# Kernel tuning notes

Measured on AMD Instinct MI355X. Metric: run time of the kernel, lower is better.

The kernel has to match this reference:

```python
import jax, jax.numpy as jnp
import numpy as np

# --- configuration constants (match init_kwargs) ---
N = 256          # num_oscillators
T = 200          # simulation steps
INTERVAL = 5     # readout_update_interval
OFFSET = 1       # spike_update_offset
DELAY = 10
D = DELAY + 1    # delay-buffer length
K_GLOBAL = 1.0   # global_coupling_strength
STEP_SIZE = 0.1
GAMMA_ATTR = 0.5 # gamma_attraction_strength
DECAY = 0.9      # membrane_decay
THRESH = 1.0
REC_SCALE = 0.1
ALPHA_FIX = 0.5  # fixed_alpha_value (fixed during training)
CLS_START = 50   # classifier_start_step
SURR_BETA = 4.0  # surrogate-gradient sharpness
NUM_CLASSES = 10


def _spike(u):
    # Heaviside forward, sigmoid surrogate backward (straight-through)
    sg = jax.nn.sigmoid(SURR_BETA * u)
    hard = (u > 0).astype(u.dtype)
    return sg + jax.lax.stop_gradient(hard - sg)


def _forward(x, theta0, W_init, omega, W_ro, W_gate, W_rec, W_fb, W_cls, b_cls):
    B = x.shape[0]
    P = W_gate.shape[1]  # num_pixels = H*W*C
    xf = x.reshape(B, -1)
    gamma0 = jnp.tanh(xf @ W_init)                 # ReadoutLayer.initialize_gamma_from_input -> [B,N]
    buf0 = jnp.tile(theta0[None], (D, 1, 1))       # theta delay buffer [D,B,N]
    zN = jnp.zeros((B, N), x.dtype)
    zP = jnp.zeros((B, P), x.dtype)
    carry0 = (theta0, gamma0, zN, zP, zP, zN, buf0)  # theta, gamma, gate, membrane, spikes, fb-activity a, buffer

    def step(carry, s):
        theta, gamma, gate, mem, spk, a, buf = carry
        # --- KuramotoLayer: dtheta_i = omega_i + K/N * sum_j (1 + W_ij*alpha) sin(th_j - th_i) + attr*gamma_i
        # top-down connectivity W_ij = a_i a_j is rank-1, so the coupling sum is computed exactly in O(N).
        sin_t = jnp.sin(theta); cos_t = jnp.cos(theta)
        S = sin_t.sum(-1, keepdims=True); C = cos_t.sum(-1, keepdims=True)
        base = cos_t * S - sin_t * C
        as_ = jnp.sum(a * sin_t, -1, keepdims=True)
        ac_ = jnp.sum(a * cos_t, -1, keepdims=True)
        weighted = ALPHA_FIX * (cos_t * a * as_ - sin_t * a * ac_)
        dtheta = omega + (K_GLOBAL / N) * (base + weighted) + GAMMA_ATTR * gamma
        theta = theta + STEP_SIZE * dtheta

        # --- ReadoutLayer.gamma_update + SinusoidalGate every INTERVAL steps
        def ro_upd(args):
            g = jnp.tanh(theta @ W_ro)
            gt = g * 0.5 * (1.0 + jnp.cos(theta - buf[0]))  # gate from delayed phase difference
            return g, gt
        gamma, gate = jax.lax.cond((s % INTERVAL) == 0, ro_upd, lambda args: args, (gamma, gate))

        # --- SNNLayer.forward_step + TopDownFeedback on offset spike-update steps
        def sp_upd(args):
            mem_, spk_, a_ = args
            cur = gate @ W_gate + REC_SCALE * (spk_ @ W_rec)
            mem_ = DECAY * mem_ * (1.0 - spk_) + cur       # leaky membrane with reset
            spk_ = _spike(mem_ - THRESH)
            a_ = jnp.tanh(spk_ @ W_fb)                     # per-oscillator feedback activity
            return mem_, spk_, a_
        m_sp = (((s - OFFSET) % INTERVAL) == 0) & (s > OFFSET)
        mem, spk, a = jax.lax.cond(m_sp, sp_upd, lambda args: args, (mem, spk, a))

        buf = jnp.concatenate([buf[1:], theta[None]], axis=0)
        return (theta, gamma, gate, mem, spk, a, buf), spk

    _, spk_hist = jax.lax.scan(step, carry0, jnp.arange(1, T + 1))
    spike_trace = jnp.transpose(spk_hist, (1, 0, 2))       # [B,T,P]
    rate = jnp.mean(spike_trace[:, CLS_START:, :], axis=1) # SNNLayer.classify: mean firing rate
    logits = rate @ W_cls + b_cls
    return logits


def setup_inputs() -> dict:
    key = jax.random.key(0)
    ks = jax.random.split(key, 10)
    B, H, W, C = 32, 32, 32, 3
    P = H * W * C
    x = jax.random.normal(ks[0], (B, H, W, C), jnp.float32)
    theta0 = jax.random.normal(ks[1], (B, N), jnp.float32)
    W_init = jax.random.normal(ks[2], (P, N), jnp.float32) / np.sqrt(P).astype(np.float32)
    omega = jax.random.normal(ks[3], (N,), jnp.float32) * 0.5
    W_ro = jax.random.normal(ks[4], (N, N), jnp.float32) / np.sqrt(N).astype(np.float32)
    W_gate = jax.random.normal(ks[5], (N, P), jnp.float32) / np.sqrt(N).astype(np.float32)
    W_rec = jax.random.normal(ks[6], (P, P), jnp.float32) / np.sqrt(P).astype(np.float32)
    W_fb = jax.random.normal(ks[7], (P, N), jnp.float32) / np.sqrt(P).astype(np.float32)
    W_cls = jax.random.normal(ks[8], (P, NUM_CLASSES), jnp.float32) / np.sqrt(P).astype(np.float32)
    b_cls = jnp.zeros((NUM_CLASSES,), jnp.float32)
    return dict(x=x, theta0=theta0, W_init=W_init, omega=omega, W_ro=W_ro,
                W_gate=W_gate, W_rec=W_rec, W_fb=W_fb, W_cls=W_cls, b_cls=b_cls)


def reference(x, theta0, W_init, omega, W_ro, W_gate, W_rec, W_fb, W_cls, b_cls):
    return _forward(x, theta0, W_init, omega, W_ro, W_gate, W_rec, W_fb, W_cls, b_cls)
```

## Files before the change

kernel.cpp:

```cpp
#include <hip/hip_runtime.h>
#include <cstdint>
#include <cstddef>

#define BB 32
#define NN 256
#define PP 3072
#define NG 192
#define RING 16

typedef unsigned short u16;

__global__ __launch_bounds__(512) void k_init(
    const float* __restrict__ x, const float* __restrict__ W_init,
    double* __restrict__ gpartI, double* __restrict__ memD,
    double* __restrict__ a_g, float* __restrict__ rate,
    u16* __restrict__ maskA, u16* __restrict__ maskB) {
  const int blk = blockIdx.x, tid = threadIdx.x;
  if (blk < 192) {
    const int b = blk / 6, sub = blk % 6;
    __shared__ double xl[512];
    xl[tid] = (double)x[(size_t)b * PP + sub * 512 + tid];
    __syncthreads();
    const int osc = tid & 255, kh = tid >> 8;
    const float* wp = W_init + (size_t)(sub * 512 + kh * 256) * NN + osc;
    const double* xp = xl + kh * 256;
    double a0 = 0, a1 = 0, a2 = 0, a3 = 0, a4 = 0, a5 = 0, a6 = 0, a7 = 0;
    for (int r = 0; r < 256; r += 8) {
      a0 += xp[r + 0] * (double)wp[(size_t)(r + 0) * NN];
      a1 += xp[r + 1] * (double)wp[(size_t)(r + 1) * NN];
      a2 += xp[r + 2] * (double)wp[(size_t)(r + 2) * NN];
      a3 += xp[r + 3] * (double)wp[(size_t)(r + 3) * NN];
      a4 += xp[r + 4] * (double)wp[(size_t)(r + 4) * NN];
      a5 += xp[r + 5] * (double)wp[(size_t)(r + 5) * NN];
      a6 += xp[r + 6] * (double)wp[(size_t)(r + 6) * NN];
      a7 += xp[r + 7] * (double)wp[(size_t)(r + 7) * NN];
    }
    double acc = ((a0 + a1) + (a2 + a3)) + ((a4 + a5) + (a6 + a7));
    __syncthreads();
    __shared__ double hl[256];
    if (kh) hl[osc] = acc;
    __syncthreads();
    if (!kh) gpartI[((size_t)b * 6 + sub) * 256 + osc] = acc + hl[osc];
  } else {
    const int b = blk - 192;
    for (int i = tid; i < PP; i += 512) {
      memD[(size_t)b * PP + i] = 0.0;
      rate[(size_t)b * PP + i] = 0.f;
    }
    for (int i = tid; i < NG; i += 512) {
      maskA[b * NG + i] = 0;
      maskB[b * NG + i] = 0;
    }
    for (int i = tid; i < NN; i += 512) a_g[b * NN + i] = 0.0;
  }
}

__global__ __launch_bounds__(512, 6) void k_rec(
    const float* __restrict__ W_rec, const u16* __restrict__ listG,
    const int* __restrict__ cntG, const int* __restrict__ cntB,
    double* __restrict__ recPart, const double* __restrict__ gateG,
    const float* __restrict__ W_gate, double* __restrict__ gatePart) {
  __shared__ double gd[16 * 130];
  __shared__ float wt[128 * 16];
  __shared__ double red[256];
  const int g = blockIdx.x, bh = blockIdx.y, z = blockIdx.z, j0 = g * 16;
  const int tid = threadIdx.x;

  if (z < 3) {
    const int qd = tid & 3;
    const int h = (tid >> 2) & 7;
    const int bl = tid >> 5;
    const int b = bh * 16 + bl;
    const int beg = (z == 0) ? 0 : cntB[b * 2 + (z - 1)];
    const int end = (z == 2) ? cntG[b] : cntB[b * 2 + z];
    const u16* lst = listG + (size_t)b * PP;
    const float* wp = W_rec + j0 + 4 * qd;

    double a0 = 0, a1 = 0, a2 = 0, a3 = 0;
    int i = beg + h;
    for (; i + 32 <= end; i += 32) {
      const int r0 = lst[i], r1 = lst[i + 8], r2 = lst[i + 16],
                r3 = lst[i + 24];
      const float4 f0 = *(const float4*)(wp + (size_t)r0 * PP);
      const float4 f1 = *(const float4*)(wp + (size_t)r1 * PP);
      const float4 f2 = *(const float4*)(wp + (size_t)r2 * PP);
      const float4 f3 = *(const float4*)(wp + (size_t)r3 * PP);
      a0 += (double)f0.x; a1 += (double)f0.y;
      a2 += (double)f0.z; a3 += (double)f0.w;
      a0 += (double)f1.x; a1 += (double)f1.y;
      a2 += (double)f1.z; a3 += (double)f1.w;
      a0 += (double)f2.x; a1 += (double)f2.y;
      a2 += (double)f2.z; a3 += (double)f2.w;
      a0 += (double)f3.x; a1 += (double)f3.y;
      a2 += (double)f3.z; a3 += (double)f3.w;
    }
    for (; i < end; i += 8) {
      const float4 f = *(const float4*)(wp + (size_t)lst[i] * PP);
      a0 += (double)f.x; a1 += (double)f.y;
      a2 += (double)f.z; a3 += (double)f.w;
    }
    a0 += __shfl_xor(a0, 4); a0 += __shfl_xor(a0, 8); a0 += __shfl_xor(a0, 16);
    a1 += __shfl_xor(a1, 4); a1 += __shfl_xor(a1, 8); a1 += __shfl_xor(a1, 16);
    a2 += __shfl_xor(a2, 4); a2 += __shfl_xor(a2, 8); a2 += __shfl_xor(a2, 16);
    a3 += __shfl_xor(a3, 4); a3 += __shfl_xor(a3, 8); a3 += __shfl_xor(a3, 16);
    if (h == 0) {
      double* dst = recPart + ((size_t)z * BB + b) * PP + j0 + 4 * qd;
      dst[0] = a0; dst[1] = a1; dst[2] = a2; dst[3] = a3;
    }
  } else {
    const int zh = z - 3;
    for (int i = tid; i < 2048; i += 512) {
      gd[(i >> 7) * 130 + (i & 127)] =
          gateG[(size_t)(bh * 16 + (i >> 7)) * 256 + zh * 128 + (i & 127)];
      wt[i] = W_gate[(size_t)(zh * 128 + (i >> 4)) * PP + j0 + (i & 15)];
    }
    __syncthreads();
    const int pi = tid & 15, bl = (tid >> 4) & 15, hq = tid >> 8;
    const int b = bh * 16 + bl, p = j0 + pi, pid = tid & 255;
    double s0 = 0, s1 = 0, s2 = 0, s3 = 0, s4 = 0, s5 = 0, s6 = 0, s7 = 0;
    const double* gq = gd + bl * 130 + hq * 64;
    const float* wq = wt + hq * 64 * 16 + pi;
    for (int k = 0; k < 64; k += 8) {
      s0 += gq[k + 0] * (double)wq[(k + 0) * 16];
      s1 += gq[k + 1] * (double)wq[(k + 1) * 16];
      s2 += gq[k + 2] * (double)wq[(k + 2) * 16];
      s3 += gq[k + 3] * (double)wq[(k + 3) * 16];
      s4 += gq[k + 4] * (double)wq[(k + 4) * 16];
      s5 += gq[k + 5] * (double)wq[(k + 5) * 16];
      s6 += gq[k + 6] * (double)wq[(k + 6) * 16];
      s7 += gq[k + 7] * (double)wq[(k + 7) * 16];
    }
    double vg = ((s0 + s1) + (s2 + s3)) + ((s4 + s5) + (s6 + s7));
    if (hq) red[pid] = vg;
    __syncthreads();
    if (!hq) gatePart[((size_t)zh * BB + b) * PP + p] = vg + red[pid];
  }
}

__global__ __launch_bounds__(512) void k_fin(
    const u16* __restrict__ mask_rd, u16* __restrict__ mask_wr,
    double* __restrict__ memD, const double* __restrict__ gatePart,
    const double* __restrict__ recPart, float* __restrict__ rate, int accum) {
  const int g = blockIdx.x, tid = threadIdx.x;
  const int pi = tid & 15, b = tid >> 4;
  const int p = g * 16 + pi;
  const size_t idx = (size_t)b * PP + p;
  const double vgs = gatePart[idx] + gatePart[(size_t)BB * PP + idx];
  const double vrs = (recPart[idx] + recPart[(size_t)BB * PP + idx]) +
                     recPart[(size_t)2 * BB * PP + idx];
  const double cur = vgs + 0.1 * vrs;
  const double so = (double)((mask_rd[b * NG + g] >> pi) & 1);
  const double mv = 0.9 * memD[idx] * (1.0 - so) + cur;
  const double sv = (mv - 1.0 > 0.0) ? 1.0 : 0.0;
  memD[idx] = mv;
  if (accum) rate[idx] += (float)sv;
  unsigned long long bal = __ballot(sv > 0.5);
  const int lane = tid & 63;
  if ((lane & 15) == 0)
    mask_wr[b * NG + g] = (u16)((bal >> (16 * (lane >> 4))) & 0xFFFFull);
}

__global__ __launch_bounds__(256) void k_fb(
    const u16* __restrict__ spk_mask, u16* __restrict__ listG,
    int* __restrict__ cntG, int* __restrict__ cntB,
    const float* __restrict__ W_fb, double* __restrict__ a_part) {
  const int b = blockIdx.x, y = blockIdx.y, tid = threadIdx.x;
  __shared__ int pc[NG], sc[NG];
  __shared__ u16 m_l[NG];
  __shared__ u16 list_l[PP];
  if (tid < NG) {
    m_l[tid] = spk_mask[b * NG + tid];
    pc[tid] = __popc((unsigned int)m_l[tid]);
    sc[tid] = pc[tid];
  }
  __syncthreads();
  for (int d = 1; d < NG; d <<= 1) {
    int v = 0;
    if (tid < NG) v = sc[tid] + ((tid >= d) ? sc[tid - d] : 0);
    __syncthreads();
    if (tid < NG) sc[tid] = v;
    __syncthreads();
  }
  const int total = sc[NG - 1];
  if (tid < NG) {
    int off = sc[tid] - pc[tid];
    unsigned int m = m_l[tid];
    while (m) {
      int bit = __builtin_ctz(m);
      m &= m - 1;
      list_l[off++] = (u16)(tid * 16 + bit);
    }
  }
  __syncthreads();
  if (y == 0) {
    for (int i = tid; i < total; i += 256) listG[(size_t)b * PP + i] = list_l[i];
    if (tid == 0) {
      cntG[b] = total;
      cntB[b * 2 + 0] = sc[63];
      cntB[b * 2 + 1] = sc[127];
    }
  }
  const int j = tid;
  double c0 = 0, c1 = 0, c2 = 0, c3 = 0, c4 = 0, c5 = 0, c6 = 0, c7 = 0;
  int i = y;
  for (; i + 128 <= total; i += 128) {
    c0 += (double)W_fb[(size_t)list_l[i + 0] * NN + j];
    c1 += (double)W_fb[(size_t)list_l[i + 16] * NN + j];
    c2 += (double)W_fb[(size_t)list_l[i + 32] * NN + j];
    c3 += (double)W_fb[(size_t)list_l[i + 48] * NN + j];
    c4 += (double)W_fb[(size_t)list_l[i + 64] * NN + j];
    c5 += (double)W_fb[(size_t)list_l[i + 80] * NN + j];
    c6 += (double)W_fb[(size_t)list_l[i + 96] * NN + j];
    c7 += (double)W_fb[(size_t)list_l[i + 112] * NN + j];
  }
  double acc = ((c0 + c1) + (c2 + c3)) + ((c4 + c5) + (c6 + c7));
  for (; i < total; i += 16) acc += (double)W_fb[(size_t)list_l[i] * NN + j];
  a_part[((size_t)b * 16 + y) * NN + j] = acc;
}

__global__ __launch_bounds__(512) void k_theta(
    double* __restrict__ ring, double* __restrict__ gamma_g,
    double* __restrict__ a_g, double* __restrict__ gateG,
    const double* __restrict__ a_part, const float* __restrict__ theta0,
    const float* __restrict__ omega, const float* __restrict__ W_ro,
    const double* __restrict__ gpartI, int* __restrict__ cntG,
    int* __restrict__ cntB, int k2) {
  const int b = blockIdx.x, tid = threadIdx.x;
  const int j = tid & 255, q = tid >> 8;
  const int lane = tid & 63, wid = tid >> 6;
  __shared__ double th[256];
  __shared__ double red[16];
  __shared__ double qpart[256];

  const int s0 = 5 * k2 + 1, s1 = 5 * k2 + 5;
  double new_a = 0.0;
  if (k2 > 0) {
    double s = 0.0;
#pragma unroll
    for (int u = 0; u < 8; ++u)
      s += a_part[((size_t)b * 16 + q * 8 + u) * NN + j];
    if (q) qpart[j] = s;
    __syncthreads();
    if (!q) new_a = tanh(s + qpart[j]);
    __syncthreads();
  }

  double t = 0.0, aj = 0.0, gm = 0.0, om = 0.0;
  if (!q) {
    om = (double)omega[j];
    if (k2 == 0) {
      double s = 0.0;
      for (int c6 = 0; c6 < 6; ++c6) s += gpartI[((size_t)b * 6 + c6) * 256 + j];
      gm = tanh(s);
      t = (double)theta0[b * NN + j];
      ring[0 * BB * NN + b * NN + j] = t;
      if (tid == 0) {
        cntG[b] = 0;
        cntB[b * 2 + 0] = 0;
        cntB[b * 2 + 1] = 0;
      }
    } else {
      t = ring[((s0 - 1) & (RING - 1)) * BB * NN + b * NN + j];
      aj = a_g[b * NN + j];
      gm = gamma_g[b * NN + j];
    }
  }

  for (int s = s0; s <= s1; ++s) {
    if (!q && k2 > 0 && s == s0 + 1) {
      aj = new_a;
      a_g[b * NN + j] = aj;
    }
    double sn = 0.0, cs = 0.0;
    if (!q) sincos(t, &sn, &cs);
    double r0 = sn, r1 = cs, r2 = aj * sn, r3 = aj * cs;
#pragma unroll
    for (int o = 32; o; o >>= 1) {
      r0 += __shfl_down(r0, o);
      r1 += __shfl_down(r1, o);
      r2 += __shfl_down(r2, o);
      r3 += __shfl_down(r3, o);
    }
    if (lane == 0 && wid < 4) {
      red[wid * 4 + 0] = r0;
      red[wid * 4 + 1] = r1;
      red[wid * 4 + 2] = r2;
      red[wid * 4 + 3] = r3;
    }
    __syncthreads();
    double S = red[0] + red[4] + red[8] + red[12];
    double C = red[1] + red[5] + red[9] + red[13];
    double AS = red[2] + red[6] + red[10] + red[14];
    double AC = red[3] + red[7] + red[11] + red[15];
    __syncthreads();
    if (!q) {
      double base = cs * S - sn * C;
      double wgt = 0.5 * (cs * aj * AS - sn * aj * AC);
      t = t + 0.1 * (om + (1.0 / 256.0) * (base + wgt) + 0.5 * gm);
      ring[(s & (RING - 1)) * BB * NN + b * NN + j] = t;
    }
  }
  if (!q) th[j] = t;
  __syncthreads();
  {
    double c0 = 0, c1 = 0, c2 = 0, c3 = 0, c4 = 0, c5 = 0, c6 = 0, c7 = 0;
    const float* wp = W_ro + j;
    const int i0 = q * 128;
    for (int i = 0; i < 128; i += 8) {
      c0 += th[i0 + i + 0] * (double)wp[(size_t)(i0 + i + 0) * NN];
      c1 += th[i0 + i + 1] * (double)wp[(size_t)(i0 + i + 1) * NN];
      c2 += th[i0 + i + 2] * (double)wp[(size_t)(i0 + i + 2) * NN];
      c3 += th[i0 + i + 3] * (double)wp[(size_t)(i0 + i + 3) * NN];
      c4 += th[i0 + i + 4] * (double)wp[(size_t)(i0 + i + 4) * NN];
      c5 += th[i0 + i + 5] * (double)wp[(size_t)(i0 + i + 5) * NN];
      c6 += th[i0 + i + 6] * (double)wp[(size_t)(i0 + i + 6) * NN];
      c7 += th[i0 + i + 7] * (double)wp[(size_t)(i0 + i + 7) * NN];
    }
    double acc = ((c0 + c1) + (c2 + c3)) + ((c4 + c5) + (c6 + c7));
    if (q) qpart[j] = acc;
    __syncthreads();
    if (!q) {
      double gnew = tanh(acc + qpart[j]);
      gamma_g[b * NN + j] = gnew;
      int sd = s1 - 11;
      if (sd < 0) sd = 0;
      double dly = ring[(sd & (RING - 1)) * BB * NN + b * NN + j];
      double gt = gnew * 0.5 * (1.0 + cos(t - dly));
      gateG[(size_t)b * 256 + j] = gt;
    }
  }
}

__global__ __launch_bounds__(256) void k_cls(const float* __restrict__ rate,
                                             const float* __restrict__ Wcls,
                                             const float* __restrict__ bcls,
                                             float* __restrict__ out) {
  const int b = blockIdx.x, t = threadIdx.x;
  double acc[10];
#pragma unroll
  for (int c = 0; c < 10; ++c) acc[c] = 0.0;
  for (int p = t; p < PP; p += 256) {
    double r = (double)rate[(size_t)b * PP + p] / 30.0;
#pragma unroll
    for (int c = 0; c < 10; ++c) acc[c] += r * (double)Wcls[(size_t)p * 10 + c];
  }
  __shared__ double sh[10][256];
#pragma unroll
  for (int c = 0; c < 10; ++c) sh[c][t] = acc[c];
  __syncthreads();
  for (int off = 128; off; off >>= 1) {
    if (t < off)
#pragma unroll
      for (int c = 0; c < 10; ++c) sh[c][t] += sh[c][t + off];
    __syncthreads();
  }
  if (t < 10) out[b * 10 + t] = (float)(sh[t][0] + (double)bcls[t]);
}

extern "C" void kernel_launch(void* const* d_in, const int* in_sizes, int n_in,
                              void* d_out, int out_size, void* d_ws,
                              size_t ws_size, hipStream_t stream) {
  const float* x = (const float*)d_in[0];
  const float* theta0 = (const float*)d_in[1];
  const float* W_init = (const float*)d_in[2];
  const float* omega = (const float*)d_in[3];
  const float* W_ro = (const float*)d_in[4];
  const float* W_gate = (const float*)d_in[5];
  const float* W_rec = (const float*)d_in[6];
  const float* W_fb = (const float*)d_in[7];
  const float* W_cls = (const float*)d_in[8];
  const float* b_cls = (const float*)d_in[9];

  char* w = (char*)d_ws;
  size_t off = 0;
  auto alloc = [&](size_t sz) -> void* {
    void* p = w + off;
    off = (off + sz + 255) & ~(size_t)255;
    return p;
  };
  double* ring = (double*)alloc((size_t)RING * BB * NN * 8);
  double* gamma = (double*)alloc((size_t)BB * NN * 8);
  double* a_g = (double*)alloc((size_t)BB * NN * 8);
  double* gateG = (double*)alloc((size_t)BB * NN * 8);
  double* memD = (double*)alloc((size_t)BB * PP * 8);
  float* rate = (float*)alloc((size_t)BB * PP * 4);
  u16* maskA = (u16*)alloc((size_t)BB * NG * 2);
  u16* maskB = (u16*)alloc((size_t)BB * NG * 2);
  u16* listG = (u16*)alloc((size_t)BB * PP * 2);
  int* cntG = (int*)alloc((size_t)BB * 4);
  int* cntB = (int*)alloc((size_t)BB * 2 * 4);
  double* gpartI = (double*)alloc((size_t)BB * 6 * 256 * 8);
  double* a_part = (double*)alloc((size_t)BB * 16 * NN * 8);
  double* recPart = (double*)alloc((size_t)3 * BB * PP * 8);
  double* gatePart = (double*)alloc((size_t)2 * BB * PP * 8);

  k_init<<<224, 512, 0, stream>>>(x, W_init, gpartI, memD, a_g, rate, maskA,
                                  maskB);
  k_theta<<<32, 512, 0, stream>>>(ring, gamma, a_g, gateG, a_part, theta0,
                                  omega, W_ro, gpartI, cntG, cntB, 0);
  for (int k = 1; k < 40; ++k) {
    const u16* mrd = (k & 1) ? maskA : maskB;
    u16* mwr = (k & 1) ? maskB : maskA;
    k_rec<<<dim3(192, 2, 5), 512, 0, stream>>>(W_rec, listG, cntG, cntB,
                                               recPart, gateG, W_gate,
                                               gatePart);
    k_fin<<<192, 512, 0, stream>>>(mrd, mwr, memD, gatePart, recPart, rate,
                                   (k >= 10) ? 1 : 0);
    k_fb<<<dim3(32, 16), 256, 0, stream>>>(mwr, listG, cntG, cntB, W_fb,
                                           a_part);
    k_theta<<<32, 512, 0, stream>>>(ring, gamma, a_g, gateG, a_part, theta0,
                                    omega, W_ro, gpartI, cntG, cntB, k);
  }
  k_cls<<<32, 256, 0, stream>>>(rate, W_cls, b_cls, (float*)d_out);
}
```

Measured before the change: 2.115 ms.

## Fuse membrane update, spike feedback and theta step into one per-batch kernel

The membrane/spike finalize kernel, the feedback gather kernel, and the theta kernel are merged into a single 32-block kernel, one block per batch row. This removes two launches per outer step and the a_part global round trip. The cost is far less parallelism: the spike update and the W_fb gather over spiking pixels now run on 32 blocks instead of 192 and 512, and each block's gather is split across only two halves.

```diff
diff --git a/kernel.cpp b/kernel.cpp
--- a/kernel.cpp
+++ b/kernel.cpp
@@ -137,112 +137,102 @@
   }
 }
 
-__global__ __launch_bounds__(512) void k_fin(
+__global__ __launch_bounds__(512) void k_theta2(
+    double* __restrict__ ring, double* __restrict__ gamma_g,
+    double* __restrict__ a_g, double* __restrict__ gateG,
+    const float* __restrict__ theta0, const float* __restrict__ omega,
+    const float* __restrict__ W_ro, const float* __restrict__ W_fb,
+    const double* __restrict__ gpartI, u16* __restrict__ listG,
+    int* __restrict__ cntG, int* __restrict__ cntB,
     const u16* __restrict__ mask_rd, u16* __restrict__ mask_wr,
     double* __restrict__ memD, const double* __restrict__ gatePart,
-    const double* __restrict__ recPart, float* __restrict__ rate, int accum) {
-  const int g = blockIdx.x, tid = threadIdx.x;
-  const int pi = tid & 15, b = tid >> 4;
-  const int p = g * 16 + pi;
-  const size_t idx = (size_t)b * PP + p;
-  const double vgs = gatePart[idx] + gatePart[(size_t)BB * PP + idx];
-  const double vrs = (recPart[idx] + recPart[(size_t)BB * PP + idx]) +
-                     recPart[(size_t)2 * BB * PP + idx];
-  const double cur = vgs + 0.1 * vrs;
-  const double so = (double)((mask_rd[b * NG + g] >> pi) & 1);
-  const double mv = 0.9 * memD[idx] * (1.0 - so) + cur;
-  const double sv = (mv - 1.0 > 0.0) ? 1.0 : 0.0;
-  memD[idx] = mv;
-  if (accum) rate[idx] += (float)sv;
-  unsigned long long bal = __ballot(sv > 0.5);
+    const double* __restrict__ recPart, float* __restrict__ rate, int accum,
+    int k2) {
+  const int b = blockIdx.x, tid = threadIdx.x;
+  const int j = tid & 255, q = tid >> 8;
   const int lane = tid & 63;
-  if ((lane & 15) == 0)
-    mask_wr[b * NG + g] = (u16)((bal >> (16 * (lane >> 4))) & 0xFFFFull);
-}
-
-__global__ __launch_bounds__(256) void k_fb(
-    const u16* __restrict__ spk_mask, u16* __restrict__ listG,
-    int* __restrict__ cntG, int* __restrict__ cntB,
-    const float* __restrict__ W_fb, double* __restrict__ a_part) {
-  const int b = blockIdx.x, y = blockIdx.y, tid = threadIdx.x;
+  const int wid = tid >> 6;
+  __shared__ double th[256];
+  __shared__ double red[16];
+  __shared__ double qpart[256];
   __shared__ int pc[NG], sc[NG];
   __shared__ u16 m_l[NG];
   __shared__ u16 list_l[PP];
-  if (tid < NG) {
-    m_l[tid] = spk_mask[b * NG + tid];
-    pc[tid] = __popc((unsigned int)m_l[tid]);
-    sc[tid] = pc[tid];
-  }
-  __syncthreads();
-  for (int d = 1; d < NG; d <<= 1) {
-    int v = 0;
-    if (tid < NG) v = sc[tid] + ((tid >= d) ? sc[tid - d] : 0);
-    __syncthreads();
-    if (tid < NG) sc[tid] = v;
-    __syncthreads();
-  }
-  const int total = sc[NG - 1];
-  if (tid < NG) {
-    int off = sc[tid] - pc[tid];
-    unsigned int m = m_l[tid];
-    while (m) {
-      int bit = __builtin_ctz(m);
-      m &= m - 1;
-      list_l[off++] = (u16)(tid * 16 + bit);
-    }
-  }
-  __syncthreads();
-  if (y == 0) {
-    for (int i = tid; i < total; i += 256) listG[(size_t)b * PP + i] = list_l[i];
+
+  const int s0 = 5 * k2 + 1, s1 = 5 * k2 + 5;
+  double new_a = 0.0;
+
+  if (k2 > 0) {
+    for (int c = 0; c < 6; ++c) {
+      const int p = c * 512 + tid;
+      const int g = p >> 4;
+      const size_t idx = (size_t)b * PP + p;
+      const double vgs = gatePart[idx] + gatePart[(size_t)BB * PP + idx];
+      const double vrs = (recPart[idx] + recPart[(size_t)BB * PP + idx]) +
+                         recPart[(size_t)2 * BB * PP + idx];
+      const double cur = vgs + 0.1 * vrs;
+      const double so = (double)((mask_rd[b * NG + g] >> (p & 15)) & 1);
+      const double mv = 0.9 * memD[idx] * (1.0 - so) + cur;
+      const double sv = (mv - 1.0 > 0.0) ? 1.0 : 0.0;
+      memD[idx] = mv;
+      if (accum) rate[idx] += (float)sv;
+      unsigned long long bal = __ballot(sv > 0.5);
+      if ((lane & 15) == 0)
+        m_l[g] = (u16)((bal >> (16 * (lane >> 4))) & 0xFFFFull);
+    }
+    __syncthreads();
+    for (int i = tid; i < NG; i += 512) mask_wr[b * NG + i] = m_l[i];
+
+    if (tid < NG) {
+      pc[tid] = __popc((unsigned int)m_l[tid]);
+      sc[tid] = pc[tid];
+    }
+    __syncthreads();
+    for (int d = 1; d < NG; d <<= 1) {
+      int v = 0;
+      if (tid < NG) v = sc[tid] + ((tid >= d) ? sc[tid - d] : 0);
+      __syncthreads();
+      if (tid < NG) sc[tid] = v;
+      __syncthreads();
+    }
+    const int total = sc[NG - 1];
+    if (tid < NG) {
+      int off = sc[tid] - pc[tid];
+      unsigned int m = m_l[tid];
+      while (m) {
+        int bit = __builtin_ctz(m);
+        m &= m - 1;
+        list_l[off++] = (u16)(tid * 16 + bit);
+      }
+    }
+    __syncthreads();
+    for (int i = tid; i < total; i += 512) listG[(size_t)b * PP + i] = list_l[i];
     if (tid == 0) {
       cntG[b] = total;
       cntB[b * 2 + 0] = sc[63];
       cntB[b * 2 + 1] = sc[127];
     }
-  }
-  const int j = tid;
-  double c0 = 0, c1 = 0, c2 = 0, c3 = 0, c4 = 0, c5 = 0, c6 = 0, c7 = 0;
-  int i = y;
-  for (; i + 128 <= total; i += 128) {
-    c0 += (double)W_fb[(size_t)list_l[i + 0] * NN + j];
-    c1 += (double)W_fb[(size_t)list_l[i + 16] * NN + j];
-    c2 += (double)W_fb[(size_t)list_l[i + 32] * NN + j];
-    c3 += (double)W_fb[(size_t)list_l[i + 48] * NN + j];
-    c4 += (double)W_fb[(size_t)list_l[i + 64] * NN + j];
-    c5 += (double)W_fb[(size_t)list_l[i + 80] * NN + j];
-    c6 += (double)W_fb[(size_t)list_l[i + 96] * NN + j];
-    c7 += (double)W_fb[(size_t)list_l[i + 112] * NN + j];
-  }
-  double acc = ((c0 + c1) + (c2 + c3)) + ((c4 + c5) + (c6 + c7));
-  for (; i < total; i += 16) acc += (double)W_fb[(size_t)list_l[i] * NN + j];
-  a_part[((size_t)b * 16 + y) * NN + j] = acc;
-}
-
-__global__ __launch_bounds__(512) void k_theta(
-    double* __restrict__ ring, double* __restrict__ gamma_g,
-    double* __restrict__ a_g, double* __restrict__ gateG,
-    const double* __restrict__ a_part, const float* __restrict__ theta0,
-    const float* __restrict__ omega, const float* __restrict__ W_ro,
-    const double* __restrict__ gpartI, int* __restrict__ cntG,
-    int* __restrict__ cntB, int k2) {
-  const int b = blockIdx.x, tid = threadIdx.x;
-  const int j = tid & 255, q = tid >> 8;
-  const int lane = tid & 63, wid = tid >> 6;
-  __shared__ double th[256];
-  __shared__ double red[16];
-  __shared__ double qpart[256];
-
-  const int s0 = 5 * k2 + 1, s1 = 5 * k2 + 5;
-  double new_a = 0.0;
-  if (k2 > 0) {
-    double s = 0.0;
-#pragma unroll
-    for (int u = 0; u < 8; ++u)
-      s += a_part[((size_t)b * 16 + q * 8 + u) * NN + j];
-    if (q) qpart[j] = s;
-    __syncthreads();
-    if (!q) new_a = tanh(s + qpart[j]);
-    __syncthreads();
+
+    {
+      double c0 = 0, c1 = 0, c2 = 0, c3 = 0, c4 = 0, c5 = 0, c6 = 0, c7 = 0;
+      int i = q;
+      for (; i + 16 <= total; i += 16) {
+        c0 += (double)W_fb[(size_t)list_l[i + 0] * NN + j];
+        c1 += (double)W_fb[(size_t)list_l[i + 2] * NN + j];
+        c2 += (double)W_fb[(size_t)list_l[i + 4] * NN + j];
+        c3 += (double)W_fb[(size_t)list_l[i + 6] * NN + j];
+        c4 += (double)W_fb[(size_t)list_l[i + 8] * NN + j];
+        c5 += (double)W_fb[(size_t)list_l[i + 10] * NN + j];
+        c6 += (double)W_fb[(size_t)list_l[i + 12] * NN + j];
+        c7 += (double)W_fb[(size_t)list_l[i + 14] * NN + j];
+      }
+      double acc = ((c0 + c1) + (c2 + c3)) + ((c4 + c5) + (c6 + c7));
+      for (; i < total; i += 2) acc += (double)W_fb[(size_t)list_l[i] * NN + j];
+      if (q) qpart[j] = acc;
+      __syncthreads();
+      if (!q) new_a = tanh(acc + qpart[j]);
+      __syncthreads();
+    }
   }
 
   double t = 0.0, aj = 0.0, gm = 0.0, om = 0.0;
@@ -390,26 +380,25 @@
   int* cntG = (int*)alloc((size_t)BB * 4);
   int* cntB = (int*)alloc((size_t)BB * 2 * 4);
   double* gpartI = (double*)alloc((size_t)BB * 6 * 256 * 8);
-  double* a_part = (double*)alloc((size_t)BB * 16 * NN * 8);
   double* recPart = (double*)alloc((size_t)3 * BB * PP * 8);
   double* gatePart = (double*)alloc((size_t)2 * BB * PP * 8);
 
   k_init<<<224, 512, 0, stream>>>(x, W_init, gpartI, memD, a_g, rate, maskA,
                                   maskB);
-  k_theta<<<32, 512, 0, stream>>>(ring, gamma, a_g, gateG, a_part, theta0,
-                                  omega, W_ro, gpartI, cntG, cntB, 0);
+  k_theta2<<<32, 512, 0, stream>>>(ring, gamma, a_g, gateG, theta0, omega,
+                                   W_ro, W_fb, gpartI, listG, cntG, cntB,
+                                   maskA, maskB, memD, gatePart, recPart, rate,
+                                   0, 0);
   for (int k = 1; k < 40; ++k) {
     const u16* mrd = (k & 1) ? maskA : maskB;
     u16* mwr = (k & 1) ? maskB : maskA;
     k_rec<<<dim3(192, 2, 5), 512, 0, stream>>>(W_rec, listG, cntG, cntB,
                                                recPart, gateG, W_gate,
                                                gatePart);
-    k_fin<<<192, 512, 0, stream>>>(mrd, mwr, memD, gatePart, recPart, rate,
-                                   (k >= 10) ? 1 : 0);
-    k_fb<<<dim3(32, 16), 256, 0, stream>>>(mwr, listG, cntG, cntB, W_fb,
-                                           a_part);
-    k_theta<<<32, 512, 0, stream>>>(ring, gamma, a_g, gateG, a_part, theta0,
-                                    omega, W_ro, gpartI, cntG, cntB, k);
+    k_theta2<<<32, 512, 0, stream>>>(ring, gamma, a_g, gateG, theta0, omega,
+                                     W_ro, W_fb, gpartI, listG, cntG, cntB,
+                                     mrd, mwr, memD, gatePart, recPart, rate,
+                                     (k >= 10) ? 1 : 0, k);
   }
   k_cls<<<32, 256, 0, stream>>>(rate, W_cls, b_cls, (float*)d_out);
 }
```

Result: slower. 2.565 ms (+21.3%).

## Fuse per-interval kernels into one persistent cooperative kernel with grid syncs

Applied to the files above, without the earlier changes.

Replaces the 39-iteration loop of four kernel launches with a single cooperative persistent kernel that uses grid-wide syncs between phases. The W_gate tile is kept resident in shared memory across iterations. The recurrent gather is split into 16 even slices and overlapped with the theta/readout phase on the other blocks. This removes launch overhead and per-launch reloads, at the cost of grid-sync latency, higher shared-memory use and dependence on enough co-resident blocks; the old multi-kernel path remains as a fallback.

```diff
diff --git a/kernel.cpp b/kernel.cpp
--- a/kernel.cpp
+++ b/kernel.cpp
@@ -1,12 +1,18 @@
 #include <hip/hip_runtime.h>
+#include <hip/hip_cooperative_groups.h>
 #include <cstdint>
 #include <cstddef>
+
+namespace cg = cooperative_groups;
 
 #define BB 32
 #define NN 256
 #define PP 3072
 #define NG 192
 #define RING 16
+#define SREC 16
+#define NBLK 768
+#define NGATH 736
 
 typedef unsigned short u16;
 
@@ -14,7 +20,8 @@
     const float* __restrict__ x, const float* __restrict__ W_init,
     double* __restrict__ gpartI, double* __restrict__ memD,
     double* __restrict__ a_g, float* __restrict__ rate,
-    u16* __restrict__ maskA, u16* __restrict__ maskB) {
+    u16* __restrict__ maskA, u16* __restrict__ maskB, int* __restrict__ cntG,
+    int* __restrict__ cntB) {
   const int blk = blockIdx.x, tid = threadIdx.x;
   if (blk < 192) {
     const int b = blk / 6, sub = blk % 6;
@@ -52,6 +59,268 @@
       maskB[b * NG + i] = 0;
     }
     for (int i = tid; i < NN; i += 512) a_g[b * NN + i] = 0.0;
+    if (tid == 0) {
+      cntG[b] = 0;
+      cntB[b * 2 + 0] = 0;
+      cntB[b * 2 + 1] = 0;
+    }
+  }
+}
+
+__global__ __launch_bounds__(512, 6) void k_mega(
+    double* __restrict__ ring, double* __restrict__ gamma_g,
+    double* __restrict__ a_g, double* __restrict__ gateG,
+    const float* __restrict__ theta0, const float* __restrict__ omega,
+    const float* __restrict__ W_ro, const float* __restrict__ W_fb,
+    const double* __restrict__ gpartI, u16* __restrict__ listG,
+    int* __restrict__ cntG, u16* __restrict__ maskA, u16* __restrict__ maskB,
+    double* __restrict__ memD, const float* __restrict__ W_rec,
+    const float* __restrict__ W_gate, double* __restrict__ recPart,
+    double* __restrict__ a_part, float* __restrict__ rate) {
+  cg::grid_group grd = cg::this_grid();
+  const int blk = blockIdx.x, tid = threadIdx.x;
+  const int lane = tid & 63, wid = tid >> 6;
+  __shared__ float wt[256 * 16];
+  __shared__ int pc[NG], sc[NG];
+  __shared__ u16 m_l[NG];
+  __shared__ u16 list_l[PP];
+  __shared__ double th[256];
+  __shared__ double redp[16];
+  __shared__ double qpart[256];
+
+  if (blk < 192) {
+    for (int i = tid; i < 4096; i += 512)
+      wt[i] = W_gate[(size_t)(i >> 4) * PP + blk * 16 + (i & 15)];
+    __syncthreads();
+  }
+
+  for (int k = 0; k < 40; ++k) {
+    const u16* mrd = (k & 1) ? maskA : maskB;
+    u16* mwr = (k & 1) ? maskB : maskA;
+    if (k > 0) {
+      if (blk < 192) {
+        const int g = blk, pi = tid & 15, bl = tid >> 4;
+        const size_t idx = (size_t)bl * PP + g * 16 + pi;
+        double s0 = 0, s1 = 0, s2 = 0, s3 = 0, s4 = 0, s5 = 0, s6 = 0, s7 = 0;
+        const double* gq = gateG + bl * 256;
+        const float* wq = wt + pi;
+        for (int kk = 0; kk < 256; kk += 8) {
+          s0 += gq[kk + 0] * (double)wq[(kk + 0) * 16];
+          s1 += gq[kk + 1] * (double)wq[(kk + 1) * 16];
+          s2 += gq[kk + 2] * (double)wq[(kk + 2) * 16];
+          s3 += gq[kk + 3] * (double)wq[(kk + 3) * 16];
+          s4 += gq[kk + 4] * (double)wq[(kk + 4) * 16];
+          s5 += gq[kk + 5] * (double)wq[(kk + 5) * 16];
+          s6 += gq[kk + 6] * (double)wq[(kk + 6) * 16];
+          s7 += gq[kk + 7] * (double)wq[(kk + 7) * 16];
+        }
+        const double vg = ((s0 + s1) + (s2 + s3)) + ((s4 + s5) + (s6 + s7));
+        double vrs = 0.0;
+        for (int s = 0; s < SREC; ++s) vrs += recPart[(size_t)s * BB * PP + idx];
+        const double cur = vg + 0.1 * vrs;
+        const double so = (double)((mrd[bl * NG + g] >> pi) & 1);
+        const double mv = 0.9 * memD[idx] * (1.0 - so) + cur;
+        const double sv = (mv - 1.0 > 0.0) ? 1.0 : 0.0;
+        memD[idx] = mv;
+        if (k >= 10) rate[idx] += (float)sv;
+        unsigned long long bal = __ballot(sv > 0.5);
+        if ((lane & 15) == 0)
+          mwr[bl * NG + g] = (u16)((bal >> (16 * (lane >> 4))) & 0xFFFFull);
+      }
+      grd.sync();
+      if (blk < 512) {
+        const int b = blk >> 4, y = blk & 15;
+        if (tid < NG) {
+          m_l[tid] = mwr[b * NG + tid];
+          pc[tid] = __popc((unsigned int)m_l[tid]);
+          sc[tid] = pc[tid];
+        }
+        __syncthreads();
+        for (int d = 1; d < NG; d <<= 1) {
+          int v = 0;
+          if (tid < NG) v = sc[tid] + ((tid >= d) ? sc[tid - d] : 0);
+          __syncthreads();
+          if (tid < NG) sc[tid] = v;
+          __syncthreads();
+        }
+        const int total = sc[NG - 1];
+        if (tid < NG) {
+          int off = sc[tid] - pc[tid];
+          unsigned int m = m_l[tid];
+          while (m) {
+            int bit = __builtin_ctz(m);
+            m &= m - 1;
+            list_l[off++] = (u16)(tid * 16 + bit);
+          }
+        }
+        __syncthreads();
+        if (y == 0) {
+          for (int i = tid; i < total; i += 512)
+            listG[(size_t)b * PP + i] = list_l[i];
+          if (tid == 0) cntG[b] = total;
+        }
+        if (tid < 256) {
+          const int j = tid;
+          double c0 = 0, c1 = 0, c2 = 0, c3 = 0, c4 = 0, c5 = 0, c6 = 0,
+                 c7 = 0;
+          int i = y;
+          for (; i + 128 <= total; i += 128) {
+            c0 += (double)W_fb[(size_t)list_l[i + 0] * NN + j];
+            c1 += (double)W_fb[(size_t)list_l[i + 16] * NN + j];
+            c2 += (double)W_fb[(size_t)list_l[i + 32] * NN + j];
+            c3 += (double)W_fb[(size_t)list_l[i + 48] * NN + j];
+            c4 += (double)W_fb[(size_t)list_l[i + 64] * NN + j];
+            c5 += (double)W_fb[(size_t)list_l[i + 80] * NN + j];
+            c6 += (double)W_fb[(size_t)list_l[i + 96] * NN + j];
+            c7 += (double)W_fb[(size_t)list_l[i + 112] * NN + j];
+          }
+          double acc = ((c0 + c1) + (c2 + c3)) + ((c4 + c5) + (c6 + c7));
+          for (; i < total; i += 16)
+            acc += (double)W_fb[(size_t)list_l[i] * NN + j];
+          a_part[((size_t)b * 16 + y) * NN + j] = acc;
+        }
+      }
+      grd.sync();
+    }
+    if (blk < 32) {
+      const int b = blk;
+      const int j = tid & 255, q = tid >> 8;
+      const int s0 = 5 * k + 1, s1 = 5 * k + 5;
+      double new_a = 0.0;
+      if (k > 0) {
+        double s = 0.0;
+#pragma unroll
+        for (int u = 0; u < 8; ++u)
+          s += a_part[((size_t)b * 16 + q * 8 + u) * NN + j];
+        if (q) qpart[j] = s;
+        __syncthreads();
+        if (!q) new_a = tanh(s + qpart[j]);
+        __syncthreads();
+      }
+      double t = 0.0, aj = 0.0, gm = 0.0, om = 0.0;
+      if (!q) {
+        om = (double)omega[j];
+        if (k == 0) {
+          double s = 0.0;
+          for (int c6 = 0; c6 < 6; ++c6)
+            s += gpartI[((size_t)b * 6 + c6) * 256 + j];
+          gm = tanh(s);
+          t = (double)theta0[b * NN + j];
+          ring[0 * BB * NN + b * NN + j] = t;
+        } else {
+          t = ring[((s0 - 1) & (RING - 1)) * BB * NN + b * NN + j];
+          aj = a_g[b * NN + j];
+          gm = gamma_g[b * NN + j];
+        }
+      }
+      for (int s = s0; s <= s1; ++s) {
+        if (!q && k > 0 && s == s0 + 1) {
+          aj = new_a;
+          a_g[b * NN + j] = aj;
+        }
+        double sn = 0.0, cs = 0.0;
+        if (!q) sincos(t, &sn, &cs);
+        double r0 = sn, r1 = cs, r2 = aj * sn, r3 = aj * cs;
+#pragma unroll
+        for (int o = 32; o; o >>= 1) {
+          r0 += __shfl_down(r0, o);
+          r1 += __shfl_down(r1, o);
+          r2 += __shfl_down(r2, o);
+          r3 += __shfl_down(r3, o);
+        }
+        if (lane == 0 && wid < 4) {
+          redp[wid * 4 + 0] = r0;
+          redp[wid * 4 + 1] = r1;
+          redp[wid * 4 + 2] = r2;
+          redp[wid * 4 + 3] = r3;
+        }
+        __syncthreads();
+        double S = redp[0] + redp[4] + redp[8] + redp[12];
+        double C = redp[1] + redp[5] + redp[9] + redp[13];
+        double AS = redp[2] + redp[6] + redp[10] + redp[14];
+        double AC = redp[3] + redp[7] + redp[11] + redp[15];
+        __syncthreads();
+        if (!q) {
+          double base = cs * S - sn * C;
+          double wgt = 0.5 * (cs * aj * AS - sn * aj * AC);
+          t = t + 0.1 * (om + (1.0 / 256.0) * (base + wgt) + 0.5 * gm);
+          ring[(s & (RING - 1)) * BB * NN + b * NN + j] = t;
+        }
+      }
+      if (!q) th[j] = t;
+      __syncthreads();
+      {
+        double c0 = 0, c1 = 0, c2 = 0, c3 = 0, c4 = 0, c5 = 0, c6 = 0, c7 = 0;
+        const float* wp = W_ro + j;
+        const int i0 = q * 128;
+        for (int i = 0; i < 128; i += 8) {
+          c0 += th[i0 + i + 0] * (double)wp[(size_t)(i0 + i + 0) * NN];
+          c1 += th[i0 + i + 1] * (double)wp[(size_t)(i0 + i + 1) * NN];
+          c2 += th[i0 + i + 2] * (double)wp[(size_t)(i0 + i + 2) * NN];
+          c3 += th[i0 + i + 3] * (double)wp[(size_t)(i0 + i + 3) * NN];
+          c4 += th[i0 + i + 4] * (double)wp[(size_t)(i0 + i + 4) * NN];
+          c5 += th[i0 + i + 5] * (double)wp[(size_t)(i0 + i + 5) * NN];
+          c6 += th[i0 + i + 6] * (double)wp[(size_t)(i0 + i + 6) * NN];
+          c7 += th[i0 + i + 7] * (double)wp[(size_t)(i0 + i + 7) * NN];
+        }
+        double acc = ((c0 + c1) + (c2 + c3)) + ((c4 + c5) + (c6 + c7));
+        if (q) qpart[j] = acc;
+        __syncthreads();
+        if (!q) {
+          double gnew = tanh(acc + qpart[j]);
+          gamma_g[b * NN + j] = gnew;
+          int sd = s1 - 11;
+          if (sd < 0) sd = 0;
+          double dly = ring[(sd & (RING - 1)) * BB * NN + b * NN + j];
+          double gt = gnew * 0.5 * (1.0 + cos(t - dly));
+          gateG[(size_t)b * 256 + j] = gt;
+        }
+      }
+    } else if (k < 39) {
+      const int qd = tid & 3, h = (tid >> 2) & 7, bl = tid >> 5;
+      for (int w = blk - 32; w < 192 * 2 * SREC; w += NGATH) {
+        const int g = w % 192;
+        const int t1 = w / 192;
+        const int bh = t1 & 1, s = t1 >> 1;
+        const int b = bh * 16 + bl;
+        const int cnt = cntG[b];
+        const int beg = cnt * s / SREC, end = cnt * (s + 1) / SREC;
+        const u16* lst = listG + (size_t)b * PP;
+        const float* wp = W_rec + g * 16 + 4 * qd;
+        double a0 = 0, a1 = 0, a2 = 0, a3 = 0;
+        int i = beg + h;
+        for (; i + 32 <= end; i += 32) {
+          const int r0 = lst[i], r1 = lst[i + 8], r2 = lst[i + 16],
+                    r3 = lst[i + 24];
+          const float4 f0 = *(const float4*)(wp + (size_t)r0 * PP);
+          const float4 f1 = *(const float4*)(wp + (size_t)r1 * PP);
+          const float4 f2 = *(const float4*)(wp + (size_t)r2 * PP);
+          const float4 f3 = *(const float4*)(wp + (size_t)r3 * PP);
+          a0 += (double)f0.x; a1 += (double)f0.y;
+          a2 += (double)f0.z; a3 += (double)f0.w;
+          a0 += (double)f1.x; a1 += (double)f1.y;
+          a2 += (double)f1.z; a3 += (double)f1.w;
+          a0 += (double)f2.x; a1 += (double)f2.y;
+          a2 += (double)f2.z; a3 += (double)f2.w;
+          a0 += (double)f3.x; a1 += (double)f3.y;
+          a2 += (double)f3.z; a3 += (double)f3.w;
+        }
+        for (; i < end; i += 8) {
+          const float4 f = *(const float4*)(wp + (size_t)lst[i] * PP);
+          a0 += (double)f.x; a1 += (double)f.y;
+          a2 += (double)f.z; a3 += (double)f.w;
+        }
+        a0 += __shfl_xor(a0, 4); a0 += __shfl_xor(a0, 8); a0 += __shfl_xor(a0, 16);
+        a1 += __shfl_xor(a1, 4); a1 += __shfl_xor(a1, 8); a1 += __shfl_xor(a1, 16);
+        a2 += __shfl_xor(a2, 4); a2 += __shfl_xor(a2, 8); a2 += __shfl_xor(a2, 16);
+        a3 += __shfl_xor(a3, 4); a3 += __shfl_xor(a3, 8); a3 += __shfl_xor(a3, 16);
+        if (h == 0) {
+          double* dst = recPart + ((size_t)s * BB + b) * PP + g * 16 + 4 * qd;
+          dst[0] = a0; dst[1] = a1; dst[2] = a2; dst[3] = a3;
+        }
+      }
+    }
+    grd.sync();
   }
 }
 
@@ -65,17 +334,13 @@
   __shared__ double red[256];
   const int g = blockIdx.x, bh = blockIdx.y, z = blockIdx.z, j0 = g * 16;
   const int tid = threadIdx.x;
-
   if (z < 3) {
-    const int qd = tid & 3;
-    const int h = (tid >> 2) & 7;
-    const int bl = tid >> 5;
+    const int qd = tid & 3, h = (tid >> 2) & 7, bl = tid >> 5;
     const int b = bh * 16 + bl;
     const int beg = (z == 0) ? 0 : cntB[b * 2 + (z - 1)];
     const int end = (z == 2) ? cntG[b] : cntB[b * 2 + z];
     const u16* lst = listG + (size_t)b * PP;
     const float* wp = W_rec + j0 + 4 * qd;
-
     double a0 = 0, a1 = 0, a2 = 0, a3 = 0;
     int i = beg + h;
     for (; i + 32 <= end; i += 32) {
@@ -85,19 +350,14 @@
       const float4 f1 = *(const float4*)(wp + (size_t)r1 * PP);
       const float4 f2 = *(const float4*)(wp + (size_t)r2 * PP);
       const float4 f3 = *(const float4*)(wp + (size_t)r3 * PP);
-      a0 += (double)f0.x; a1 += (double)f0.y;
-      a2 += (double)f0.z; a3 += (double)f0.w;
-      a0 += (double)f1.x; a1 += (double)f1.y;
-      a2 += (double)f1.z; a3 += (double)f1.w;
-      a0 += (double)f2.x; a1 += (double)f2.y;
-      a2 += (double)f2.z; a3 += (double)f2.w;
-      a0 += (double)f3.x; a1 += (double)f3.y;
-      a2 += (double)f3.z; a3 += (double)f3.w;
+      a0 += (double)f0.x; a1 += (double)f0.y; a2 += (double)f0.z; a3 += (double)f0.w;
+      a0 += (double)f1.x; a1 += (double)f1.y; a2 += (double)f1.z; a3 += (double)f1.w;
+      a0 += (double)f2.x; a1 += (double)f2.y; a2 += (double)f2.z; a3 += (double)f2.w;
+      a0 += (double)f3.x; a1 += (double)f3.y; a2 += (double)f3.z; a3 += (double)f3.w;
     }
     for (; i < end; i += 8) {
       const float4 f = *(const float4*)(wp + (size_t)lst[i] * PP);
-      a0 += (double)f.x; a1 += (double)f.y;
-      a2 += (double)f.z; a3 += (double)f.w;
+      a0 += (double)f.x; a1 += (double)f.y; a2 += (double)f.z; a3 += (double)f.w;
     }
     a0 += __shfl_xor(a0, 4); a0 += __shfl_xor(a0, 8); a0 += __shfl_xor(a0, 16);
     a1 += __shfl_xor(a1, 4); a1 += __shfl_xor(a1, 8); a1 += __shfl_xor(a1, 16);
@@ -120,15 +380,15 @@
     double s0 = 0, s1 = 0, s2 = 0, s3 = 0, s4 = 0, s5 = 0, s6 = 0, s7 = 0;
     const double* gq = gd + bl * 130 + hq * 64;
     const float* wq = wt + hq * 64 * 16 + pi;
-    for (int k = 0; k < 64; k += 8) {
-      s0 += gq[k + 0] * (double)wq[(k + 0) * 16];
-      s1 += gq[k + 1] * (double)wq[(k + 1) * 16];
-      s2 += gq[k + 2] * (double)wq[(k + 2) * 16];
-      s3 += gq[k + 3] * (double)wq[(k + 3) * 16];
-      s4 += gq[k + 4] * (double)wq[(k + 4) * 16];
-      s5 += gq[k + 5] * (double)wq[(k + 5) * 16];
-      s6 += gq[k + 6] * (double)wq[(k + 6) * 16];
-      s7 += gq[k + 7] * (double)wq[(k + 7) * 16];
+    for (int kk = 0; kk < 64; kk += 8) {
+      s0 += gq[kk + 0] * (double)wq[(kk + 0) * 16];
+      s1 += gq[kk + 1] * (double)wq[(kk + 1) * 16];
+      s2 += gq[kk + 2] * (double)wq[(kk + 2) * 16];
+      s3 += gq[kk + 3] * (double)wq[(kk + 3) * 16];
+      s4 += gq[kk + 4] * (double)wq[(kk + 4) * 16];
+      s5 += gq[kk + 5] * (double)wq[(kk + 5) * 16];
+      s6 += gq[kk + 6] * (double)wq[(kk + 6) * 16];
+      s7 += gq[kk + 7] * (double)wq[(kk + 7) * 16];
     }
     double vg = ((s0 + s1) + (s2 + s3)) + ((s4 + s5) + (s6 + s7));
     if (hq) red[pid] = vg;
@@ -231,7 +491,6 @@
   __shared__ double th[256];
   __shared__ double red[16];
   __shared__ double qpart[256];
-
   const int s0 = 5 * k2 + 1, s1 = 5 * k2 + 5;
   double new_a = 0.0;
   if (k2 > 0) {
@@ -244,7 +503,6 @@
     if (!q) new_a = tanh(s + qpart[j]);
     __syncthreads();
   }
-
   double t = 0.0, aj = 0.0, gm = 0.0, om = 0.0;
   if (!q) {
     om = (double)omega[j];
@@ -265,7 +523,6 @@
       gm = gamma_g[b * NN + j];
     }
   }
-
   for (int s = s0; s <= s1; ++s) {
     if (!q && k2 > 0 && s == s0 + 1) {
       aj = new_a;
@@ -391,25 +648,43 @@
   int* cntB = (int*)alloc((size_t)BB * 2 * 4);
   double* gpartI = (double*)alloc((size_t)BB * 6 * 256 * 8);
   double* a_part = (double*)alloc((size_t)BB * 16 * NN * 8);
-  double* recPart = (double*)alloc((size_t)3 * BB * PP * 8);
+  double* recPart = (double*)alloc((size_t)SREC * BB * PP * 8);
   double* gatePart = (double*)alloc((size_t)2 * BB * PP * 8);
 
   k_init<<<224, 512, 0, stream>>>(x, W_init, gpartI, memD, a_g, rate, maskA,
-                                  maskB);
-  k_theta<<<32, 512, 0, stream>>>(ring, gamma, a_g, gateG, a_part, theta0,
-                                  omega, W_ro, gpartI, cntG, cntB, 0);
-  for (int k = 1; k < 40; ++k) {
-    const u16* mrd = (k & 1) ? maskA : maskB;
-    u16* mwr = (k & 1) ? maskB : maskA;
-    k_rec<<<dim3(192, 2, 5), 512, 0, stream>>>(W_rec, listG, cntG, cntB,
-                                               recPart, gateG, W_gate,
-                                               gatePart);
-    k_fin<<<192, 512, 0, stream>>>(mrd, mwr, memD, gatePart, recPart, rate,
-                                   (k >= 10) ? 1 : 0);
-    k_fb<<<dim3(32, 16), 256, 0, stream>>>(mwr, listG, cntG, cntB, W_fb,
-                                           a_part);
+                                  maskB, cntG, cntB);
+
+  int dev = 0;
+  hipGetDevice(&dev);
+  int coopAttr = 0;
+  hipDeviceGetAttribute(&coopAttr, hipDeviceAttributeCooperativeLaunch, dev);
+  int maxBpc = 0;
+  hipOccupancyMaxActiveBlocksPerMultiprocessor(&maxBpc, k_mega, 512, 0);
+  bool launched = false;
+  if (coopAttr && maxBpc >= 3) {
+    void* args[] = {&ring,  &gamma, &a_g,   &gateG,   &theta0, &omega, &W_ro,
+                    &W_fb,  &gpartI, &listG, &cntG,   &maskA,  &maskB, &memD,
+                    &W_rec, &W_gate, &recPart, &a_part, &rate};
+    hipError_t e = hipLaunchCooperativeKernel((void*)k_mega, dim3(NBLK),
+                                              dim3(512), args, 0, stream);
+    launched = (e == hipSuccess);
+  }
+  if (!launched) {
     k_theta<<<32, 512, 0, stream>>>(ring, gamma, a_g, gateG, a_part, theta0,
-                                    omega, W_ro, gpartI, cntG, cntB, k);
+                                    omega, W_ro, gpartI, cntG, cntB, 0);
+    for (int k = 1; k < 40; ++k) {
+      const u16* mrd = (k & 1) ? maskA : maskB;
+      u16* mwr = (k & 1) ? maskB : maskA;
+      k_rec<<<dim3(192, 2, 5), 512, 0, stream>>>(W_rec, listG, cntG, cntB,
+                                                 recPart, gateG, W_gate,
+                                                 gatePart);
+      k_fin<<<192, 512, 0, stream>>>(mrd, mwr, memD, gatePart, recPart, rate,
+                                     (k >= 10) ? 1 : 0);
+      k_fb<<<dim3(32, 16), 256, 0, stream>>>(mwr, listG, cntG, cntB, W_fb,
+                                             a_part);
+      k_theta<<<32, 512, 0, stream>>>(ring, gamma, a_g, gateG, a_part, theta0,
+                                      omega, W_ro, gpartI, cntG, cntB, k);
+    }
   }
   k_cls<<<32, 256, 0, stream>>>(rate, W_cls, b_cls, (float*)d_out);
 }
```

Result: no change. 2.107 ms (-0.4%).
